# Optimization experiments

Measured on AMD Instinct MI355X. Metric: run time of the kernel, lower is better.

## Reference

```python
import jax, jax.numpy as jnp
import numpy as np

DIM = 256
NUM_HEADS = 4
HEAD_DIM = DIM // NUM_HEADS
SCALE = HEAD_DIM ** -0.5


def setup_inputs() -> dict:
    key = jax.random.key(0)
    ks = jax.random.split(key, 11)
    B, Nq, Nkv = 4, 2048, 2048
    inp = {
        "query_feat": jax.random.normal(ks[0], (B, Nq, DIM), dtype=jnp.float32),
        "key_value_feat": jax.random.normal(ks[1], (B, Nkv, DIM), dtype=jnp.float32),
        "reliability_kv": jax.random.uniform(ks[2], (B, Nkv), dtype=jnp.float32),
        "Wq": jax.random.normal(ks[3], (DIM, DIM), dtype=jnp.float32) * (DIM ** -0.5),
        "bq": jnp.zeros((DIM,), jnp.float32),
        "Wk": jax.random.normal(ks[4], (DIM, DIM), dtype=jnp.float32) * (DIM ** -0.5),
        "bk": jnp.zeros((DIM,), jnp.float32),
        "Wv": jax.random.normal(ks[5], (DIM, DIM), dtype=jnp.float32) * (DIM ** -0.5),
        "bv": jnp.zeros((DIM,), jnp.float32),
        "Wo": jax.random.normal(ks[6], (DIM, DIM), dtype=jnp.float32) * (DIM ** -0.5),
        "bo": jnp.zeros((DIM,), jnp.float32),
    }
    return inp


def _heads(x):
    B, N, C = x.shape
    return x.reshape(B, N, NUM_HEADS, HEAD_DIM).transpose(0, 2, 1, 3)  # [B,H,N,hd]


def reference(query_feat, key_value_feat, reliability_kv, Wq, bq, Wk, bk, Wv, bv, Wo, bo):
    B, Nq, _ = query_feat.shape
    q = _heads(query_feat @ Wq + bq)          # [B,H,Nq,hd]
    k = _heads(key_value_feat @ Wk + bk)      # [B,H,Nkv,hd]
    v = _heads(key_value_feat @ Wv + bv)
    # gate K/V by reliability (broadcast over heads and head_dim)
    rk = reliability_kv[:, None, :, None]     # [B,1,Nkv,1]
    k = k * rk
    v = v * rk
    attn = jnp.einsum("bhqd,bhkd->bhqk", q, k) * SCALE
    log_r = jnp.log(jnp.clip(reliability_kv, 1e-6))[:, None, None, :]  # [B,1,1,Nkv]
    attn = jax.nn.softmax(attn + log_r, axis=-1)  # [B,H,Nq,Nkv]
    out = jnp.einsum("bhqk,bhkd->bhqd", attn, v)
    out = out.transpose(0, 2, 1, 3).reshape(B, Nq, DIM)
    out = out @ Wo + bo
    attn_mean = attn.mean(axis=1)  # [B,Nq,Nkv]
    return out, attn_mean
```

## Files before the change

### kernel.cpp

```cpp
#include <hip/hip_runtime.h>


typedef __attribute__((ext_vector_type(8))) _Float16 half8;
typedef __attribute__((ext_vector_type(4))) float f32x4;

#define MFMAH(A, B, C) __builtin_amdgcn_mfma_f32_16x16x32_f16((A), (B), (C), 0, 0, 0)

__device__ __forceinline__ unsigned short f2h(float f) {
    union { _Float16 h; unsigned short u; } c; c.h = (_Float16)f; return c.u;
}
__device__ __forceinline__ float h2f(unsigned short u) {
    union { unsigned short u; _Float16 h; } c; c.u = u; return (float)c.h;
}
__device__ __forceinline__ half8 ldh8(const unsigned short* p) {
    return *reinterpret_cast<const half8*>(p);
}
__device__ __forceinline__ void gld16(const unsigned short* g, unsigned short* l) {
    __builtin_amdgcn_global_load_lds(
        (const __attribute__((address_space(1))) unsigned int*)g,
        (__attribute__((address_space(3))) unsigned int*)l, 16, 0, 0);
}

__global__ void wsplit_kernel(const float* __restrict__ Wq, const float* __restrict__ Wk,
                              const float* __restrict__ Wv, const float* __restrict__ Wo,
                              unsigned short* __restrict__ WT) {
    int e = blockIdx.x * 256 + threadIdx.x;
    int m = e >> 16;
    int idx = e & 65535;
    int k = idx >> 8, n = idx & 255;
    const float* W = (m == 0) ? Wq : (m == 1) ? Wk : (m == 2) ? Wv : Wo;
    WT[m * 65536 + n * 256 + k] = f2h(W[idx]);
}

#define STAGE_W(dst_, src_, kt_) do {                                               \
    _Pragma("unroll")                                                               \
    for (int j_ = 0; j_ < 4; ++j_) {                                                \
        int s_ = w * 4 + j_;                                                        \
        int rowl_ = 8 * s_ + (l >> 3);                                              \
        int so_ = rowl_ * 256 + (kt_) * 64 + (((l & 7) ^ (rowl_ & 7)) << 3);        \
        gld16(&(src_)[so_], &(dst_)[s_ * 512]);                                     \
    }                                                                               \
} while (0)

#define GEMM_TILE(buf_, kt_) do {                                                   \
    _Pragma("unroll")                                                               \
    for (int ksl_ = 0; ksl_ < 2; ++ksl_) {                                          \
        _Pragma("unroll")                                                           \
        for (int n_ = 0; n_ < 16; ++n_) {                                           \
            int r_ = n_ * 16 + l15;                                                 \
            int idx_ = r_ * 64 + ((((ksl_)*4 + lg) ^ (r_ & 7)) << 3);               \
            half8 b_ = ldh8(&(buf_)[idx_]);                                         \
            acc[n_] = MFMAH(ah[(kt_) * 2 + ksl_], b_, acc[n_]);                     \
        }                                                                           \
    }                                                                               \
} while (0)

__global__ __launch_bounds__(512, 1) void proj3_kernel(
    const float* __restrict__ query, const float* __restrict__ kv,
    const float* __restrict__ rel, const unsigned short* __restrict__ WT,
    const float* __restrict__ bq, const float* __restrict__ bk, const float* __restrict__ bv,
    unsigned short* __restrict__ Qh, unsigned short* __restrict__ Kh,
    unsigned short* __restrict__ Vtmp) {
    const int job = blockIdx.y;
    const float* X = (job == 0) ? query : kv;
    const unsigned short* wg = WT + job * 65536;
    const float* bias = (job == 0) ? bq : (job == 1) ? bk : bv;
    const float* rs = (job == 0) ? nullptr : rel;
    unsigned short* oh = (job == 0) ? Qh : (job == 1) ? Kh : Vtmp;

    __shared__ __align__(16) unsigned short wlds[2][256 * 64];

    const int w = threadIdx.x >> 6, l = threadIdx.x & 63;
    const int l15 = l & 15, lg = l >> 4;
    const int arow = blockIdx.x * 128 + w * 16 + l15;

    half8 ah[8];
#pragma unroll
    for (int ks = 0; ks < 8; ++ks) {
        const float* p = &X[arow * 256 + ks * 32 + lg * 8];
        float4 f0 = *reinterpret_cast<const float4*>(p);
        float4 f1 = *reinterpret_cast<const float4*>(p + 4);
        half8 t;
        t[0] = (_Float16)f0.x; t[1] = (_Float16)f0.y; t[2] = (_Float16)f0.z; t[3] = (_Float16)f0.w;
        t[4] = (_Float16)f1.x; t[5] = (_Float16)f1.y; t[6] = (_Float16)f1.z; t[7] = (_Float16)f1.w;
        ah[ks] = t;
    }
    f32x4 acc[16];
#pragma unroll
    for (int n = 0; n < 16; ++n) acc[n] = (f32x4){0.f, 0.f, 0.f, 0.f};

    STAGE_W(wlds[0], wg, 0);
    __syncthreads();
#pragma unroll
    for (int kt = 0; kt < 4; ++kt) {
        const int cur = kt & 1, nx = cur ^ 1;
        if (kt < 3) STAGE_W(wlds[nx], wg, kt + 1);
        GEMM_TILE(wlds[cur], kt);
        __syncthreads();
    }

    const int orow0 = blockIdx.x * 128 + w * 16 + lg * 4;
    float rsv[4];
#pragma unroll
    for (int r = 0; r < 4; ++r) rsv[r] = rs ? rs[orow0 + r] : 1.0f;
#pragma unroll
    for (int n = 0; n < 16; ++n) {
        const int col = n * 16 + l15;
        const float bn = bias[col];
#pragma unroll
        for (int r = 0; r < 4; ++r)
            oh[(orow0 + r) * 256 + col] = f2h((acc[n][r] + bn) * rsv[r]);
    }
}

__global__ void transpose_v_kernel(const unsigned short* __restrict__ Vtmp,
                                   unsigned short* __restrict__ Vt) {
    __shared__ unsigned short tile[32][36];
    const int b = blockIdx.z;
    const int k0 = blockIdx.x * 32, d0 = blockIdx.y * 32;
    const int t = threadIdx.x;
    {
        int kr = t >> 3, dc4 = (t & 7) * 4;
        ushort4 v = *reinterpret_cast<const ushort4*>(&Vtmp[(b * 2048 + k0 + kr) * 256 + d0 + dc4]);
        tile[kr][dc4 + 0] = v.x; tile[kr][dc4 + 1] = v.y;
        tile[kr][dc4 + 2] = v.z; tile[kr][dc4 + 3] = v.w;
    }
    __syncthreads();
    {
        int dr = t >> 3, kc4 = (t & 7) * 4;
        ushort4 o;
        o.x = tile[kc4 + 0][dr]; o.y = tile[kc4 + 1][dr];
        o.z = tile[kc4 + 2][dr]; o.w = tile[kc4 + 3][dr];
        *reinterpret_cast<ushort4*>(&Vt[(b * 256 + d0 + dr) * 2048 + k0 + kc4]) = o;
    }
}

__global__ __launch_bounds__(512, 1) void attn_pass1(
    const unsigned short* __restrict__ Qh, const unsigned short* __restrict__ Kh,
    const unsigned short* __restrict__ Vt, const float* __restrict__ rel,
    float* __restrict__ sinv_ws, unsigned short* __restrict__ AO) {
    const int bid = blockIdx.x;
    const int sw = (bid & 7) * 32 + (bid >> 3);
    const int b = sw >> 6;
    const int q0 = (sw & 63) * 32;
    const int tid = threadIdx.x;
    const int w = tid >> 6;
    const int h = w & 3, ks = w >> 2;
    const int l = tid & 63, l15 = l & 15, lg = l >> 4;
    const float C2 = 0.18033688011112042f;

    __shared__ __align__(16) unsigned short ldsK[8][2][2048];
    __shared__ __align__(16) unsigned short ldsV[8][2][2048];
    __shared__ __align__(16) unsigned short pbf[8][2][640];
    __shared__ __align__(16) unsigned short rel_h[2048];
    __shared__ float ssum_sh[2][4][2][16];

    {
        float4 v = reinterpret_cast<const float4*>(&rel[b * 2048])[tid];
        ushort4 o;
        o.x = f2h(fmaxf(v.x, 1e-6f)); o.y = f2h(fmaxf(v.y, 1e-6f));
        o.z = f2h(fmaxf(v.z, 1e-6f)); o.w = f2h(fmaxf(v.w, 1e-6f));
        *reinterpret_cast<ushort4*>(&rel_h[tid * 4]) = o;
    }

    half8 qf00, qf01, qf10, qf11;
    {
        const int o0 = (b * 2048 + q0 + l15) * 256 + h * 64 + lg * 8;
        const int o1 = (b * 2048 + q0 + 16 + l15) * 256 + h * 64 + lg * 8;
        qf00 = ldh8(&Qh[o0]); qf01 = ldh8(&Qh[o0 + 32]);
        qf10 = ldh8(&Qh[o1]); qf11 = ldh8(&Qh[o1 + 32]);
    }
    __syncthreads();

#define STAGE1(buf_, kt_) do {                                                      \
    _Pragma("unroll")                                                               \
    for (int j_ = 0; j_ < 4; ++j_) {                                                \
        int r_ = 8 * j_ + (l >> 3);                                                 \
        size_t sk_ = (size_t)(b * 2048 + (kt_) * 32 + r_) * 256 + h * 64 +          \
                     (((l & 7) ^ (l >> 3)) << 3);                                   \
        gld16(&Kh[sk_], &ldsK[w][buf_][j_ * 512]);                                  \
    }                                                                               \
    _Pragma("unroll")                                                               \
    for (int j_ = 0; j_ < 4; ++j_) {                                                \
        int d_ = 16 * j_ + (l >> 2);                                                \
        size_t sv_ = (size_t)(b * 256 + h * 64 + d_) * 2048 + (kt_) * 32 +          \
                     (((l & 3) ^ ((l >> 3) & 3)) << 3);                             \
        gld16(&Vt[sv_], &ldsV[w][buf_][j_ * 512]);                                  \
    }                                                                               \
} while (0)

    float ssum0 = 0.f, ssum1 = 0.f;
    f32x4 oacc0[4], oacc1[4];
#pragma unroll
    for (int dc = 0; dc < 4; ++dc) {
        oacc0[dc] = (f32x4){0.f, 0.f, 0.f, 0.f};
        oacc1[dc] = (f32x4){0.f, 0.f, 0.f, 0.f};
    }

    const int ktb = ks * 32;
    STAGE1(0, ktb);
    for (int i = 0; i < 32; ++i) {
        const int cur = i & 1, nx = cur ^ 1;
        if (i < 31) {
            STAGE1(nx, ktb + i + 1);
            asm volatile("s_waitcnt vmcnt(8)" ::: "memory");
        } else {
            asm volatile("s_waitcnt vmcnt(0)" ::: "memory");
        }
        __builtin_amdgcn_sched_barrier(0);
        const int kt = ktb + i;
#pragma unroll
        for (int kc = 0; kc < 2; ++kc) {
            const int r = kc * 16 + l15;
            const int rx = l15 & 7;
            half8 kf0 = ldh8(&ldsK[w][cur][r * 64 + ((lg ^ rx) << 3)]);
            half8 kf1 = ldh8(&ldsK[w][cur][r * 64 + (((4 + lg) ^ rx) << 3)]);
            f32x4 a0 = (f32x4){0.f, 0.f, 0.f, 0.f}, a1 = a0;
            a0 = MFMAH(kf0, qf00, a0); a0 = MFMAH(kf1, qf01, a0);
            a1 = MFMAH(kf0, qf10, a1); a1 = MFMAH(kf1, qf11, a1);
            float p00, p01, p02, p03, p10, p11, p12, p13;
            {
                const int kb0 = kt * 32 + kc * 16 + lg * 4;
                float rc0 = h2f(rel_h[kb0]),     rc1 = h2f(rel_h[kb0 + 1]);
                float rc2 = h2f(rel_h[kb0 + 2]), rc3 = h2f(rel_h[kb0 + 3]);
                p00 = exp2f(a0[0] * C2) * rc0; p01 = exp2f(a0[1] * C2) * rc1;
                p02 = exp2f(a0[2] * C2) * rc2; p03 = exp2f(a0[3] * C2) * rc3;
                p10 = exp2f(a1[0] * C2) * rc0; p11 = exp2f(a1[1] * C2) * rc1;
                p12 = exp2f(a1[2] * C2) * rc2; p13 = exp2f(a1[3] * C2) * rc3;
            }
            ssum0 += (p00 + p01) + (p02 + p03);
            ssum1 += (p10 + p11) + (p12 + p13);
            uint2 w0, w1;
            w0.x = (unsigned)f2h(p00) | ((unsigned)f2h(p01) << 16);
            w0.y = (unsigned)f2h(p02) | ((unsigned)f2h(p03) << 16);
            w1.x = (unsigned)f2h(p10) | ((unsigned)f2h(p11) << 16);
            w1.y = (unsigned)f2h(p12) | ((unsigned)f2h(p13) << 16);
            *reinterpret_cast<uint2*>(&pbf[w][0][l15 * 40 + kc * 16 + lg * 4]) = w0;
            *reinterpret_cast<uint2*>(&pbf[w][1][l15 * 40 + kc * 16 + lg * 4]) = w1;
        }
        {
            half8 pa0 = ldh8(&pbf[w][0][l15 * 40 + lg * 8]);
            half8 pa1 = ldh8(&pbf[w][1][l15 * 40 + lg * 8]);
#pragma unroll
            for (int dc = 0; dc < 4; ++dc) {
                const int d = dc * 16 + l15;
                half8 vf = ldh8(&ldsV[w][cur][d * 32 + ((lg ^ ((l15 >> 1) & 3)) << 3)]);
                oacc0[dc] = MFMAH(pa0, vf, oacc0[dc]);
                oacc1[dc] = MFMAH(pa1, vf, oacc1[dc]);
            }
        }
    }
#undef STAGE1

    {
        float v0 = ssum0, v1 = ssum1;
        v0 += __shfl_xor(v0, 16); v0 += __shfl_xor(v0, 32);
        v1 += __shfl_xor(v1, 16); v1 += __shfl_xor(v1, 32);
        if (lg == 0) {
            ssum_sh[ks][h][0][l15] = v0;
            ssum_sh[ks][h][1][l15] = v1;
        }
    }
    float* ob = (float*)&ldsV[4][0][0];
    if (ks == 1) {
        const int base = (h * 64 + l) * 32;
#pragma unroll
        for (int dc = 0; dc < 4; ++dc)
#pragma unroll
            for (int r4 = 0; r4 < 4; ++r4) {
                int i0 = dc * 4 + r4, i1 = 16 + dc * 4 + r4;
                ob[base + ((i0 + l) & 31)] = oacc0[dc][r4];
                ob[base + ((i1 + l) & 31)] = oacc1[dc][r4];
            }
    }
    __syncthreads();
    if (ks == 0) {
        const int base = (h * 64 + l) * 32;
        float siv0[4], siv1[4];
#pragma unroll
        for (int r4 = 0; r4 < 4; ++r4) {
            int q = lg * 4 + r4;
            siv0[r4] = 1.0f / (ssum_sh[0][h][0][q] + ssum_sh[1][h][0][q]);
            siv1[r4] = 1.0f / (ssum_sh[0][h][1][q] + ssum_sh[1][h][1][q]);
        }
#pragma unroll
        for (int dc = 0; dc < 4; ++dc)
#pragma unroll
            for (int r4 = 0; r4 < 4; ++r4) {
                int i0 = dc * 4 + r4, i1 = 16 + dc * 4 + r4;
                float t0 = (oacc0[dc][r4] + ob[base + ((i0 + l) & 31)]) * siv0[r4];
                float t1 = (oacc1[dc][r4] + ob[base + ((i1 + l) & 31)]) * siv1[r4];
                AO[(size_t)(b * 2048 + q0 + lg * 4 + r4) * 256 + h * 64 + dc * 16 + l15] = f2h(t0);
                AO[(size_t)(b * 2048 + q0 + 16 + lg * 4 + r4) * 256 + h * 64 + dc * 16 + l15] = f2h(t1);
            }
        if (l15 == 0) {
#pragma unroll
            for (int r4 = 0; r4 < 4; ++r4) {
                sinv_ws[(b * 4 + h) * 2048 + q0 + lg * 4 + r4] = siv0[r4];
                sinv_ws[(b * 4 + h) * 2048 + q0 + 16 + lg * 4 + r4] = siv1[r4];
            }
        }
    }
}

__global__ __launch_bounds__(256, 2) void attn_mean_kernel(
    const unsigned short* __restrict__ Qh, const unsigned short* __restrict__ Kh,
    const float* __restrict__ rel, const float* __restrict__ sinv_ws,
    float* __restrict__ attn_mean) {
    const int kslice = blockIdx.x >> 8;
    const int inner = blockIdx.x & 255;
    const int sw = (inner & 7) * 32 + (inner >> 3);
    const int b = sw >> 6;
    const int q0 = (sw & 63) * 32;
    const int tid = threadIdx.x;
    const int w = tid >> 6;
    const int h = w;
    const int l = tid & 63, l15 = l & 15, lg = l >> 4;
    const int kb = b * 2048;
    const float C2 = 0.18033688011112042f;

    __shared__ __align__(16) unsigned short ldsK[2][8192];
    __shared__ __align__(16) unsigned short pbf2[2][4][2][640];
    __shared__ __align__(16) unsigned short rel_h[2048];

#define STAGE_KM(dst_, kt_) do {                                                    \
    _Pragma("unroll")                                                               \
    for (int j_ = 0; j_ < 4; ++j_) {                                                \
        int s_ = w * 4 + j_;                                                        \
        int r_ = 2 * s_ + (l >> 5);                                                 \
        size_t so_ = (size_t)(kb + (kt_) * 32 + r_) * 256 +                         \
                     (((l & 31) ^ (r_ & 7)) << 3);                                  \
        gld16(&Kh[so_], &(dst_)[s_ * 512]);                                         \
    }                                                                               \
} while (0)

    {
        float4 v0 = reinterpret_cast<const float4*>(&rel[b * 2048])[tid * 2];
        float4 v1 = reinterpret_cast<const float4*>(&rel[b * 2048])[tid * 2 + 1];
        ushort4 o0, o1;
        o0.x = f2h(fmaxf(v0.x, 1e-6f)); o0.y = f2h(fmaxf(v0.y, 1e-6f));
        o0.z = f2h(fmaxf(v0.z, 1e-6f)); o0.w = f2h(fmaxf(v0.w, 1e-6f));
        o1.x = f2h(fmaxf(v1.x, 1e-6f)); o1.y = f2h(fmaxf(v1.y, 1e-6f));
        o1.z = f2h(fmaxf(v1.z, 1e-6f)); o1.w = f2h(fmaxf(v1.w, 1e-6f));
        *reinterpret_cast<ushort4*>(&rel_h[tid * 8]) = o0;
        *reinterpret_cast<ushort4*>(&rel_h[tid * 8 + 4]) = o1;
    }

    half8 qf00, qf01, qf10, qf11;
    {
        const int o0 = (b * 2048 + q0 + l15) * 256 + h * 64 + lg * 8;
        const int o1 = (b * 2048 + q0 + 16 + l15) * 256 + h * 64 + lg * 8;
        qf00 = ldh8(&Qh[o0]); qf01 = ldh8(&Qh[o0 + 32]);
        qf10 = ldh8(&Qh[o1]); qf11 = ldh8(&Qh[o1 + 32]);
    }
    const float si0 = sinv_ws[(b * 4 + h) * 2048 + q0 + l15];
    const float si1 = sinv_ws[(b * 4 + h) * 2048 + q0 + 16 + l15];

    const int kt0 = kslice * 16;
    STAGE_KM(ldsK[0], kt0);
    __syncthreads();
    for (int ki = 0; ki < 16; ++ki) {
        const int kt = kt0 + ki;
        const int cur = ki & 1, nx = cur ^ 1;
        if (ki < 15) STAGE_KM(ldsK[nx], kt + 1);
#pragma unroll
        for (int kc = 0; kc < 2; ++kc) {
            const int r = kc * 16 + l15;
            const int rx = r & 7;
            half8 kf0 = ldh8(&ldsK[cur][r * 256 + (((h * 8 + lg) ^ rx) << 3)]);
            half8 kf1 = ldh8(&ldsK[cur][r * 256 + (((h * 8 + 4 + lg) ^ rx) << 3)]);
            f32x4 a0 = (f32x4){0.f, 0.f, 0.f, 0.f}, a1 = a0;
            a0 = MFMAH(kf0, qf00, a0); a0 = MFMAH(kf1, qf01, a0);
            a1 = MFMAH(kf0, qf10, a1); a1 = MFMAH(kf1, qf11, a1);
            const int kb0 = kt * 32 + kc * 16 + lg * 4;
            float rc0 = h2f(rel_h[kb0]),     rc1 = h2f(rel_h[kb0 + 1]);
            float rc2 = h2f(rel_h[kb0 + 2]), rc3 = h2f(rel_h[kb0 + 3]);
            uint2 w0, w1;
            w0.x = (unsigned)f2h(exp2f(a0[0] * C2) * rc0 * si0) |
                   ((unsigned)f2h(exp2f(a0[1] * C2) * rc1 * si0) << 16);
            w0.y = (unsigned)f2h(exp2f(a0[2] * C2) * rc2 * si0) |
                   ((unsigned)f2h(exp2f(a0[3] * C2) * rc3 * si0) << 16);
            w1.x = (unsigned)f2h(exp2f(a1[0] * C2) * rc0 * si1) |
                   ((unsigned)f2h(exp2f(a1[1] * C2) * rc1 * si1) << 16);
            w1.y = (unsigned)f2h(exp2f(a1[2] * C2) * rc2 * si1) |
                   ((unsigned)f2h(exp2f(a1[3] * C2) * rc3 * si1) << 16);
            *reinterpret_cast<uint2*>(&pbf2[cur][h][0][l15 * 40 + kc * 16 + lg * 4]) = w0;
            *reinterpret_cast<uint2*>(&pbf2[cur][h][1][l15 * 40 + kc * 16 + lg * 4]) = w1;
        }
        __syncthreads();
        {
            const int qs_ = tid >> 7, row = (tid >> 3) & 15, kq = tid & 7;
            float m0 = 0.f, m1 = 0.f, m2 = 0.f, m3 = 0.f;
#pragma unroll
            for (int hh = 0; hh < 4; ++hh) {
                ushort4 u = *reinterpret_cast<const ushort4*>(&pbf2[cur][hh][qs_][row * 40 + kq * 4]);
                m0 += h2f(u.x); m1 += h2f(u.y); m2 += h2f(u.z); m3 += h2f(u.w);
            }
            float4 o = (float4){m0 * 0.25f, m1 * 0.25f, m2 * 0.25f, m3 * 0.25f};
            *reinterpret_cast<float4*>(
                &attn_mean[(size_t)(b * 2048 + q0 + qs_ * 16 + row) * 2048 + kt * 32 + kq * 4]) = o;
        }
    }
#undef STAGE_KM
}

__global__ __launch_bounds__(512, 1) void final_kernel(
    const unsigned short* __restrict__ AO, const unsigned short* __restrict__ WoT,
    const float* __restrict__ bo, float* __restrict__ out) {
    __shared__ __align__(16) unsigned short wlds[2][256 * 64];

    const int w = threadIdx.x >> 6, l = threadIdx.x & 63;
    const int l15 = l & 15, lg = l >> 4;
    const int arow = blockIdx.x * 128 + w * 16 + l15;

    half8 ah[8];
#pragma unroll
    for (int ks = 0; ks < 8; ++ks)
        ah[ks] = ldh8(&AO[arow * 256 + ks * 32 + lg * 8]);
    f32x4 acc[16];
#pragma unroll
    for (int n = 0; n < 16; ++n) acc[n] = (f32x4){0.f, 0.f, 0.f, 0.f};

    STAGE_W(wlds[0], WoT, 0);
    __syncthreads();
#pragma unroll
    for (int kt = 0; kt < 4; ++kt) {
        const int cur = kt & 1, nx = cur ^ 1;
        if (kt < 3) STAGE_W(wlds[nx], WoT, kt + 1);
        GEMM_TILE(wlds[cur], kt);
        __syncthreads();
    }

    const int orow0 = blockIdx.x * 128 + w * 16 + lg * 4;
#pragma unroll
    for (int n = 0; n < 16; ++n) {
        const int col = n * 16 + l15;
        const float bn = bo[col];
#pragma unroll
        for (int r = 0; r < 4; ++r)
            out[(orow0 + r) * 256 + col] = acc[n][r] + bn;
    }
}

extern "C" void kernel_launch(void* const* d_in, const int* in_sizes, int n_in,
                              void* d_out, int out_size, void* d_ws, size_t ws_size,
                              hipStream_t stream) {
    const float* query = (const float*)d_in[0];
    const float* kv    = (const float*)d_in[1];
    const float* rel   = (const float*)d_in[2];
    const float* Wq    = (const float*)d_in[3];
    const float* bq    = (const float*)d_in[4];
    const float* Wk    = (const float*)d_in[5];
    const float* bk    = (const float*)d_in[6];
    const float* Wv    = (const float*)d_in[7];
    const float* bv    = (const float*)d_in[8];
    const float* Wo    = (const float*)d_in[9];
    const float* bo    = (const float*)d_in[10];

    char* ws = (char*)d_ws;
    unsigned short* WT   = (unsigned short*)(ws + 0);
    unsigned short* Qh   = (unsigned short*)(ws + 524288);
    unsigned short* Kh   = (unsigned short*)(ws + 4718592);
    unsigned short* Vtmp = (unsigned short*)(ws + 8912896);
    unsigned short* Vt   = (unsigned short*)(ws + 13107200);
    unsigned short* AO   = (unsigned short*)(ws + 17301504);
    float*          sinv = (float*)(ws + 21495808);

    float* out = (float*)d_out;
    float* attn_mean = (float*)d_out + 2097152;

    wsplit_kernel<<<1024, 256, 0, stream>>>(Wq, Wk, Wv, Wo, WT);
    proj3_kernel<<<dim3(64, 3), 512, 0, stream>>>(query, kv, rel, WT,
                                                  bq, bk, bv, Qh, Kh, Vtmp);
    transpose_v_kernel<<<dim3(64, 8, 4), 256, 0, stream>>>(Vtmp, Vt);
    attn_pass1<<<256, 512, 0, stream>>>(Qh, Kh, Vt, rel, sinv, AO);
    attn_mean_kernel<<<1024, 256, 0, stream>>>(Qh, Kh, rel, sinv, attn_mean);
    final_kernel<<<64, 512, 0, stream>>>(AO, WT + 3 * 65536, bo, out);
}
```

Baseline: 129.3 us.

## Split attention KV range across blocks with combine kernel and restructure V layout

The attention pass now splits the KV range in two across blocks, doubling the grid to 512, writing fp32 partial outputs and row sums, and adds a combine kernel that reduces them into AO and the inverse sums. V is re-tiled into 16-key blocks so P can feed a 16x16x16 MFMA directly from registers, which removes the LDS round trip for P. Reliability is folded in as a precomputed log2 added inside exp2, with packed fp16 conversions. The attn_mean kernel is given finer k-slices and explicit waitcnt/barrier pipelining. The aim is more parallelism and less LDS traffic, at the cost of an extra kernel launch, the partial-output memory traffic, and reuse of the Vtmp buffer as scratch.

After: 123.1 us. -4.8%, faster.

```diff
diff --git a/kernel.cpp b/kernel.cpp
--- a/kernel.cpp
+++ b/kernel.cpp
@@ -2,9 +2,12 @@
 
 
 typedef __attribute__((ext_vector_type(8))) _Float16 half8;
+typedef __attribute__((ext_vector_type(4))) _Float16 half4;
+typedef __attribute__((ext_vector_type(2))) __fp16 fp16x2;
 typedef __attribute__((ext_vector_type(4))) float f32x4;
 
-#define MFMAH(A, B, C) __builtin_amdgcn_mfma_f32_16x16x32_f16((A), (B), (C), 0, 0, 0)
+#define MFMAH32(A, B, C) __builtin_amdgcn_mfma_f32_16x16x32_f16((A), (B), (C), 0, 0, 0)
+#define MFMAH16(A, B, C) __builtin_amdgcn_mfma_f32_16x16x16f16((A), (B), (C), 0, 0, 0)
 
 __device__ __forceinline__ unsigned short f2h(float f) {
     union { _Float16 h; unsigned short u; } c; c.h = (_Float16)f; return c.u;
@@ -14,6 +17,20 @@
 }
 __device__ __forceinline__ half8 ldh8(const unsigned short* p) {
     return *reinterpret_cast<const half8*>(p);
+}
+__device__ __forceinline__ half4 ldh4(const unsigned short* p) {
+    return *reinterpret_cast<const half4*>(p);
+}
+__device__ __forceinline__ half4 pk4(float a, float b, float c, float d) {
+    union { fp16x2 h2[2]; half4 h4; } u;
+    u.h2[0] = __builtin_amdgcn_cvt_pkrtz(a, b);
+    u.h2[1] = __builtin_amdgcn_cvt_pkrtz(c, d);
+    return u.h4;
+}
+__device__ __forceinline__ unsigned int pku(float a, float b) {
+    union { fp16x2 h2; unsigned int u; } c;
+    c.h2 = __builtin_amdgcn_cvt_pkrtz(a, b);
+    return c.u;
 }
 __device__ __forceinline__ void gld16(const unsigned short* g, unsigned short* l) {
     __builtin_amdgcn_global_load_lds(
@@ -50,7 +67,7 @@
             int r_ = n_ * 16 + l15;                                                 \
             int idx_ = r_ * 64 + ((((ksl_)*4 + lg) ^ (r_ & 7)) << 3);               \
             half8 b_ = ldh8(&(buf_)[idx_]);                                         \
-            acc[n_] = MFMAH(ah[(kt_) * 2 + ksl_], b_, acc[n_]);                     \
+            acc[n_] = MFMAH32(ah[(kt_) * 2 + ksl_], b_, acc[n_]);                   \
         }                                                                           \
     }                                                                               \
 } while (0)
@@ -115,192 +132,197 @@
 
 __global__ void transpose_v_kernel(const unsigned short* __restrict__ Vtmp,
                                    unsigned short* __restrict__ Vt) {
-    __shared__ unsigned short tile[32][36];
-    const int b = blockIdx.z;
-    const int k0 = blockIdx.x * 32, d0 = blockIdx.y * 32;
+    __shared__ unsigned short tile[16][264];
+    const int st = blockIdx.x, b = blockIdx.y;
     const int t = threadIdx.x;
+#pragma unroll
+    for (int it = 0; it < 4; ++it) {
+        int idx = it * 256 + t;
+        int kr = idx >> 6;
+        int d4 = (idx & 63) * 4;
+        ushort4 v = *reinterpret_cast<const ushort4*>(
+            &Vtmp[(size_t)(b * 2048 + st * 16 + kr) * 256 + d4]);
+        tile[kr][d4 + 0] = v.x; tile[kr][d4 + 1] = v.y;
+        tile[kr][d4 + 2] = v.z; tile[kr][d4 + 3] = v.w;
+    }
+    __syncthreads();
     {
-        int kr = t >> 3, dc4 = (t & 7) * 4;
-        ushort4 v = *reinterpret_cast<const ushort4*>(&Vtmp[(b * 2048 + k0 + kr) * 256 + d0 + dc4]);
-        tile[kr][dc4 + 0] = v.x; tile[kr][dc4 + 1] = v.y;
-        tile[kr][dc4 + 2] = v.z; tile[kr][dc4 + 3] = v.w;
-    }
-    __syncthreads();
-    {
-        int dr = t >> 3, kc4 = (t & 7) * 4;
-        ushort4 o;
-        o.x = tile[kc4 + 0][dr]; o.y = tile[kc4 + 1][dr];
-        o.z = tile[kc4 + 2][dr]; o.w = tile[kc4 + 3][dr];
-        *reinterpret_cast<ushort4*>(&Vt[(b * 256 + d0 + dr) * 2048 + k0 + kc4]) = o;
-    }
-}
-
-__global__ __launch_bounds__(512, 1) void attn_pass1(
+        const int d = t;
+        unsigned int u[8];
+#pragma unroll
+        for (int k2 = 0; k2 < 8; ++k2)
+            u[k2] = (unsigned int)tile[k2 * 2][d] | ((unsigned int)tile[k2 * 2 + 1][d] << 16);
+        uint4* dst = reinterpret_cast<uint4*>(&Vt[((size_t)(b * 128 + st) * 256 + d) * 16]);
+        dst[0] = (uint4){u[0], u[1], u[2], u[3]};
+        dst[1] = (uint4){u[4], u[5], u[6], u[7]};
+    }
+}
+
+__global__ __launch_bounds__(512, 4) void attn_pass1(
     const unsigned short* __restrict__ Qh, const unsigned short* __restrict__ Kh,
     const unsigned short* __restrict__ Vt, const float* __restrict__ rel,
-    float* __restrict__ sinv_ws, unsigned short* __restrict__ AO) {
+    float* __restrict__ po_a, float* __restrict__ po_b, float* __restrict__ ps) {
     const int bid = blockIdx.x;
-    const int sw = (bid & 7) * 32 + (bid >> 3);
-    const int b = sw >> 6;
-    const int q0 = (sw & 63) * 32;
+    const int sw = (bid & 7) * 64 + (bid >> 3);
+    const int b = sw >> 7;
+    const int rem = sw & 127;
+    const int kh = rem & 1;
+    const int q0 = (rem >> 1) * 32;
     const int tid = threadIdx.x;
-    const int w = tid >> 6;
-    const int h = w & 3, ks = w >> 2;
+    const int w = tid >> 6, h = w & 3, ks = w >> 2;
     const int l = tid & 63, l15 = l & 15, lg = l >> 4;
     const float C2 = 0.18033688011112042f;
 
-    __shared__ __align__(16) unsigned short ldsK[8][2][2048];
-    __shared__ __align__(16) unsigned short ldsV[8][2][2048];
-    __shared__ __align__(16) unsigned short pbf[8][2][640];
-    __shared__ __align__(16) unsigned short rel_h[2048];
+    __shared__ __align__(16) unsigned short ldsK[8][2][1024];
+    __shared__ __align__(16) unsigned short ldsV[8][2][1024];
+    __shared__ float rel_lr[2048];
     __shared__ float ssum_sh[2][4][2][16];
 
     {
         float4 v = reinterpret_cast<const float4*>(&rel[b * 2048])[tid];
-        ushort4 o;
-        o.x = f2h(fmaxf(v.x, 1e-6f)); o.y = f2h(fmaxf(v.y, 1e-6f));
-        o.z = f2h(fmaxf(v.z, 1e-6f)); o.w = f2h(fmaxf(v.w, 1e-6f));
-        *reinterpret_cast<ushort4*>(&rel_h[tid * 4]) = o;
+        float* d = &rel_lr[tid * 4];
+        d[0] = log2f(fmaxf(v.x, 1e-6f)); d[1] = log2f(fmaxf(v.y, 1e-6f));
+        d[2] = log2f(fmaxf(v.z, 1e-6f)); d[3] = log2f(fmaxf(v.w, 1e-6f));
     }
 
     half8 qf00, qf01, qf10, qf11;
     {
         const int o0 = (b * 2048 + q0 + l15) * 256 + h * 64 + lg * 8;
-        const int o1 = (b * 2048 + q0 + 16 + l15) * 256 + h * 64 + lg * 8;
+        const int o1 = o0 + 16 * 256;
         qf00 = ldh8(&Qh[o0]); qf01 = ldh8(&Qh[o0 + 32]);
         qf10 = ldh8(&Qh[o1]); qf11 = ldh8(&Qh[o1 + 32]);
     }
     __syncthreads();
 
-#define STAGE1(buf_, kt_) do {                                                      \
+    const int st0 = kh * 64 + ks * 32;
+
+#define STG(buf_, i_) do {                                                          \
+    const unsigned short* kbp_ = Kh + (size_t)(b * 2048 + (st0 + (i_)) * 16) * 256  \
+                                 + h * 64;                                          \
     _Pragma("unroll")                                                               \
-    for (int j_ = 0; j_ < 4; ++j_) {                                                \
-        int r_ = 8 * j_ + (l >> 3);                                                 \
-        size_t sk_ = (size_t)(b * 2048 + (kt_) * 32 + r_) * 256 + h * 64 +          \
-                     (((l & 7) ^ (l >> 3)) << 3);                                   \
-        gld16(&Kh[sk_], &ldsK[w][buf_][j_ * 512]);                                  \
+    for (int j_ = 0; j_ < 2; ++j_) {                                                \
+        int r_ = j_ * 8 + (l >> 3);                                                 \
+        gld16(kbp_ + r_ * 256 + (((l & 7) ^ ((l >> 3) & 7)) << 3),                  \
+              &ldsK[w][buf_][j_ * 512]);                                            \
     }                                                                               \
+    const unsigned short* vbp_ = Vt + (size_t)((b * 128 + st0 + (i_)) * 256         \
+                                 + h * 64) * 16;                                    \
     _Pragma("unroll")                                                               \
-    for (int j_ = 0; j_ < 4; ++j_) {                                                \
-        int d_ = 16 * j_ + (l >> 2);                                                \
-        size_t sv_ = (size_t)(b * 256 + h * 64 + d_) * 2048 + (kt_) * 32 +          \
-                     (((l & 3) ^ ((l >> 3) & 3)) << 3);                             \
-        gld16(&Vt[sv_], &ldsV[w][buf_][j_ * 512]);                                  \
+    for (int j_ = 0; j_ < 2; ++j_) {                                                \
+        int d_ = j_ * 32 + (l >> 1);                                                \
+        gld16(vbp_ + d_ * 16 + (((l & 1) ^ ((l >> 1) & 1)) << 3),                   \
+              &ldsV[w][buf_][j_ * 512]);                                            \
     }                                                                               \
 } while (0)
 
     float ssum0 = 0.f, ssum1 = 0.f;
-    f32x4 oacc0[4], oacc1[4];
+    f32x4 o0acc[4], o1acc[4];
 #pragma unroll
     for (int dc = 0; dc < 4; ++dc) {
-        oacc0[dc] = (f32x4){0.f, 0.f, 0.f, 0.f};
-        oacc1[dc] = (f32x4){0.f, 0.f, 0.f, 0.f};
-    }
-
-    const int ktb = ks * 32;
-    STAGE1(0, ktb);
+        o0acc[dc] = (f32x4){0.f, 0.f, 0.f, 0.f};
+        o1acc[dc] = (f32x4){0.f, 0.f, 0.f, 0.f};
+    }
+
+    STG(0, 0);
     for (int i = 0; i < 32; ++i) {
         const int cur = i & 1, nx = cur ^ 1;
         if (i < 31) {
-            STAGE1(nx, ktb + i + 1);
-            asm volatile("s_waitcnt vmcnt(8)" ::: "memory");
+            STG(nx, i + 1);
+            asm volatile("s_waitcnt vmcnt(4)" ::: "memory");
         } else {
             asm volatile("s_waitcnt vmcnt(0)" ::: "memory");
         }
         __builtin_amdgcn_sched_barrier(0);
-        const int kt = ktb + i;
-#pragma unroll
-        for (int kc = 0; kc < 2; ++kc) {
-            const int r = kc * 16 + l15;
-            const int rx = l15 & 7;
-            half8 kf0 = ldh8(&ldsK[w][cur][r * 64 + ((lg ^ rx) << 3)]);
-            half8 kf1 = ldh8(&ldsK[w][cur][r * 64 + (((4 + lg) ^ rx) << 3)]);
-            f32x4 a0 = (f32x4){0.f, 0.f, 0.f, 0.f}, a1 = a0;
-            a0 = MFMAH(kf0, qf00, a0); a0 = MFMAH(kf1, qf01, a0);
-            a1 = MFMAH(kf0, qf10, a1); a1 = MFMAH(kf1, qf11, a1);
-            float p00, p01, p02, p03, p10, p11, p12, p13;
-            {
-                const int kb0 = kt * 32 + kc * 16 + lg * 4;
-                float rc0 = h2f(rel_h[kb0]),     rc1 = h2f(rel_h[kb0 + 1]);
-                float rc2 = h2f(rel_h[kb0 + 2]), rc3 = h2f(rel_h[kb0 + 3]);
-                p00 = exp2f(a0[0] * C2) * rc0; p01 = exp2f(a0[1] * C2) * rc1;
-                p02 = exp2f(a0[2] * C2) * rc2; p03 = exp2f(a0[3] * C2) * rc3;
-                p10 = exp2f(a1[0] * C2) * rc0; p11 = exp2f(a1[1] * C2) * rc1;
-                p12 = exp2f(a1[2] * C2) * rc2; p13 = exp2f(a1[3] * C2) * rc3;
+        half8 kf0 = ldh8(&ldsK[w][cur][l15 * 64 + ((lg ^ (l15 & 7)) << 3)]);
+        half8 kf1 = ldh8(&ldsK[w][cur][l15 * 64 + (((4 + lg) ^ (l15 & 7)) << 3)]);
+        f32x4 a0 = (f32x4){0.f, 0.f, 0.f, 0.f}, a1 = a0;
+        a0 = MFMAH32(kf0, qf00, a0); a0 = MFMAH32(kf1, qf01, a0);
+        a1 = MFMAH32(kf0, qf10, a1); a1 = MFMAH32(kf1, qf11, a1);
+        float4 lr4 = *reinterpret_cast<const float4*>(&rel_lr[(st0 + i) * 16 + lg * 4]);
+        float p00 = exp2f(__builtin_fmaf(a0[0], C2, lr4.x));
+        float p01 = exp2f(__builtin_fmaf(a0[1], C2, lr4.y));
+        float p02 = exp2f(__builtin_fmaf(a0[2], C2, lr4.z));
+        float p03 = exp2f(__builtin_fmaf(a0[3], C2, lr4.w));
+        float p10 = exp2f(__builtin_fmaf(a1[0], C2, lr4.x));
+        float p11 = exp2f(__builtin_fmaf(a1[1], C2, lr4.y));
+        float p12 = exp2f(__builtin_fmaf(a1[2], C2, lr4.z));
+        float p13 = exp2f(__builtin_fmaf(a1[3], C2, lr4.w));
+        ssum0 += (p00 + p01) + (p02 + p03);
+        ssum1 += (p10 + p11) + (p12 + p13);
+        half4 pa0 = pk4(p00, p01, p02, p03);
+        half4 pa1 = pk4(p10, p11, p12, p13);
+#pragma unroll
+        for (int dc = 0; dc < 4; ++dc) {
+            const int d = dc * 16 + l15;
+            half4 vf = ldh4(&ldsV[w][cur][d * 16 + ((((lg >> 1) ^ (d & 1))) << 3) + (lg & 1) * 4]);
+            o0acc[dc] = MFMAH16(pa0, vf, o0acc[dc]);
+            o1acc[dc] = MFMAH16(pa1, vf, o1acc[dc]);
+        }
+    }
+#undef STG
+
+    float v0 = ssum0, v1 = ssum1;
+    v0 += __shfl_xor(v0, 16); v0 += __shfl_xor(v0, 32);
+    v1 += __shfl_xor(v1, 16); v1 += __shfl_xor(v1, 32);
+
+    __syncthreads();
+    if (l < 16) { ssum_sh[ks][h][0][l] = v0; ssum_sh[ks][h][1][l] = v1; }
+    float* obuf = (float*)&ldsK[0][0][0];
+    if (ks == 1) {
+#pragma unroll
+        for (int dc = 0; dc < 4; ++dc)
+#pragma unroll
+            for (int r = 0; r < 4; ++r) {
+                const int d = h * 64 + dc * 16 + l15;
+                obuf[(lg * 4 + r) * 256 + d] = o0acc[dc][r];
+                obuf[(16 + lg * 4 + r) * 256 + d] = o1acc[dc][r];
             }
-            ssum0 += (p00 + p01) + (p02 + p03);
-            ssum1 += (p10 + p11) + (p12 + p13);
-            uint2 w0, w1;
-            w0.x = (unsigned)f2h(p00) | ((unsigned)f2h(p01) << 16);
-            w0.y = (unsigned)f2h(p02) | ((unsigned)f2h(p03) << 16);
-            w1.x = (unsigned)f2h(p10) | ((unsigned)f2h(p11) << 16);
-            w1.y = (unsigned)f2h(p12) | ((unsigned)f2h(p13) << 16);
-            *reinterpret_cast<uint2*>(&pbf[w][0][l15 * 40 + kc * 16 + lg * 4]) = w0;
-            *reinterpret_cast<uint2*>(&pbf[w][1][l15 * 40 + kc * 16 + lg * 4]) = w1;
+    }
+    __syncthreads();
+    if (ks == 0) {
+        const int chunk = b * 2 + kh;
+        float* po = (chunk < 2) ? (po_a + (size_t)chunk * 524288)
+                                : (po_b + (size_t)(chunk - 2) * 524288);
+#pragma unroll
+        for (int dc = 0; dc < 4; ++dc)
+#pragma unroll
+            for (int r = 0; r < 4; ++r) {
+                const int d = h * 64 + dc * 16 + l15;
+                const int qa = lg * 4 + r, qb = 16 + lg * 4 + r;
+                po[(size_t)(q0 + qa) * 256 + d] = o0acc[dc][r] + obuf[qa * 256 + d];
+                po[(size_t)(q0 + qb) * 256 + d] = o1acc[dc][r] + obuf[qb * 256 + d];
+            }
+        if (l < 16) {
+            ps[(chunk * 4 + h) * 2048 + q0 + l] =
+                ssum_sh[0][h][0][l] + ssum_sh[1][h][0][l];
+            ps[(chunk * 4 + h) * 2048 + q0 + 16 + l] =
+                ssum_sh[0][h][1][l] + ssum_sh[1][h][1][l];
         }
-        {
-            half8 pa0 = ldh8(&pbf[w][0][l15 * 40 + lg * 8]);
-            half8 pa1 = ldh8(&pbf[w][1][l15 * 40 + lg * 8]);
-#pragma unroll
-            for (int dc = 0; dc < 4; ++dc) {
-                const int d = dc * 16 + l15;
-                half8 vf = ldh8(&ldsV[w][cur][d * 32 + ((lg ^ ((l15 >> 1) & 3)) << 3)]);
-                oacc0[dc] = MFMAH(pa0, vf, oacc0[dc]);
-                oacc1[dc] = MFMAH(pa1, vf, oacc1[dc]);
-            }
-        }
-    }
-#undef STAGE1
-
-    {
-        float v0 = ssum0, v1 = ssum1;
-        v0 += __shfl_xor(v0, 16); v0 += __shfl_xor(v0, 32);
-        v1 += __shfl_xor(v1, 16); v1 += __shfl_xor(v1, 32);
-        if (lg == 0) {
-            ssum_sh[ks][h][0][l15] = v0;
-            ssum_sh[ks][h][1][l15] = v1;
-        }
-    }
-    float* ob = (float*)&ldsV[4][0][0];
-    if (ks == 1) {
-        const int base = (h * 64 + l) * 32;
-#pragma unroll
-        for (int dc = 0; dc < 4; ++dc)
-#pragma unroll
-            for (int r4 = 0; r4 < 4; ++r4) {
-                int i0 = dc * 4 + r4, i1 = 16 + dc * 4 + r4;
-                ob[base + ((i0 + l) & 31)] = oacc0[dc][r4];
-                ob[base + ((i1 + l) & 31)] = oacc1[dc][r4];
-            }
-    }
-    __syncthreads();
-    if (ks == 0) {
-        const int base = (h * 64 + l) * 32;
-        float siv0[4], siv1[4];
-#pragma unroll
-        for (int r4 = 0; r4 < 4; ++r4) {
-            int q = lg * 4 + r4;
-            siv0[r4] = 1.0f / (ssum_sh[0][h][0][q] + ssum_sh[1][h][0][q]);
-            siv1[r4] = 1.0f / (ssum_sh[0][h][1][q] + ssum_sh[1][h][1][q]);
-        }
-#pragma unroll
-        for (int dc = 0; dc < 4; ++dc)
-#pragma unroll
-            for (int r4 = 0; r4 < 4; ++r4) {
-                int i0 = dc * 4 + r4, i1 = 16 + dc * 4 + r4;
-                float t0 = (oacc0[dc][r4] + ob[base + ((i0 + l) & 31)]) * siv0[r4];
-                float t1 = (oacc1[dc][r4] + ob[base + ((i1 + l) & 31)]) * siv1[r4];
-                AO[(size_t)(b * 2048 + q0 + lg * 4 + r4) * 256 + h * 64 + dc * 16 + l15] = f2h(t0);
-                AO[(size_t)(b * 2048 + q0 + 16 + lg * 4 + r4) * 256 + h * 64 + dc * 16 + l15] = f2h(t1);
-            }
-        if (l15 == 0) {
-#pragma unroll
-            for (int r4 = 0; r4 < 4; ++r4) {
-                sinv_ws[(b * 4 + h) * 2048 + q0 + lg * 4 + r4] = siv0[r4];
-                sinv_ws[(b * 4 + h) * 2048 + q0 + 16 + lg * 4 + r4] = siv1[r4];
-            }
-        }
-    }
+    }
+}
+
+__global__ __launch_bounds__(256) void combine_kernel(
+    const float* __restrict__ po_a, const float* __restrict__ po_b,
+    const float* __restrict__ ps, unsigned short* __restrict__ AO,
+    float* __restrict__ sinv_ws) {
+    const int t = blockIdx.x * 256 + threadIdx.x;
+    const int d4 = t & 63;
+    const int bq = t >> 6;
+    const int q = bq & 2047;
+    const int b = bq >> 11;
+    const int d0 = d4 * 4, h = d0 >> 6;
+    const int c0 = b * 2, c1 = b * 2 + 1;
+    const float* p0 = (c0 < 2) ? po_a + (size_t)c0 * 524288 : po_b + (size_t)(c0 - 2) * 524288;
+    const float* p1 = (c1 < 2) ? po_a + (size_t)c1 * 524288 : po_b + (size_t)(c1 - 2) * 524288;
+    float4 x = *reinterpret_cast<const float4*>(&p0[(size_t)q * 256 + d0]);
+    float4 y = *reinterpret_cast<const float4*>(&p1[(size_t)q * 256 + d0]);
+    float s = ps[(c0 * 4 + h) * 2048 + q] + ps[(c1 * 4 + h) * 2048 + q];
+    float si = 1.0f / s;
+    ushort4 o;
+    o.x = f2h((x.x + y.x) * si); o.y = f2h((x.y + y.y) * si);
+    o.z = f2h((x.z + y.z) * si); o.w = f2h((x.w + y.w) * si);
+    *reinterpret_cast<ushort4*>(&AO[((size_t)(b * 2048 + q)) * 256 + d0]) = o;
+    if (d4 == (h << 4)) sinv_ws[(b * 4 + h) * 2048 + q] = si;
 }
 
 __global__ __launch_bounds__(256, 2) void attn_mean_kernel(
@@ -321,7 +343,7 @@
 
     __shared__ __align__(16) unsigned short ldsK[2][8192];
     __shared__ __align__(16) unsigned short pbf2[2][4][2][640];
-    __shared__ __align__(16) unsigned short rel_h[2048];
+    __shared__ float rel_lr[2048];
 
 #define STAGE_KM(dst_, kt_) do {                                                    \
     _Pragma("unroll")                                                               \
@@ -337,32 +359,37 @@
     {
         float4 v0 = reinterpret_cast<const float4*>(&rel[b * 2048])[tid * 2];
         float4 v1 = reinterpret_cast<const float4*>(&rel[b * 2048])[tid * 2 + 1];
-        ushort4 o0, o1;
-        o0.x = f2h(fmaxf(v0.x, 1e-6f)); o0.y = f2h(fmaxf(v0.y, 1e-6f));
-        o0.z = f2h(fmaxf(v0.z, 1e-6f)); o0.w = f2h(fmaxf(v0.w, 1e-6f));
-        o1.x = f2h(fmaxf(v1.x, 1e-6f)); o1.y = f2h(fmaxf(v1.y, 1e-6f));
-        o1.z = f2h(fmaxf(v1.z, 1e-6f)); o1.w = f2h(fmaxf(v1.w, 1e-6f));
-        *reinterpret_cast<ushort4*>(&rel_h[tid * 8]) = o0;
-        *reinterpret_cast<ushort4*>(&rel_h[tid * 8 + 4]) = o1;
+        float* d = &rel_lr[tid * 8];
+        d[0] = log2f(fmaxf(v0.x, 1e-6f)); d[1] = log2f(fmaxf(v0.y, 1e-6f));
+        d[2] = log2f(fmaxf(v0.z, 1e-6f)); d[3] = log2f(fmaxf(v0.w, 1e-6f));
+        d[4] = log2f(fmaxf(v1.x, 1e-6f)); d[5] = log2f(fmaxf(v1.y, 1e-6f));
+        d[6] = log2f(fmaxf(v1.z, 1e-6f)); d[7] = log2f(fmaxf(v1.w, 1e-6f));
     }
 
     half8 qf00, qf01, qf10, qf11;
     {
         const int o0 = (b * 2048 + q0 + l15) * 256 + h * 64 + lg * 8;
-        const int o1 = (b * 2048 + q0 + 16 + l15) * 256 + h * 64 + lg * 8;
+        const int o1 = o0 + 16 * 256;
         qf00 = ldh8(&Qh[o0]); qf01 = ldh8(&Qh[o0 + 32]);
         qf10 = ldh8(&Qh[o1]); qf11 = ldh8(&Qh[o1 + 32]);
     }
-    const float si0 = sinv_ws[(b * 4 + h) * 2048 + q0 + l15];
-    const float si1 = sinv_ws[(b * 4 + h) * 2048 + q0 + 16 + l15];
-
-    const int kt0 = kslice * 16;
+    const float lsi0 = log2f(sinv_ws[(b * 4 + h) * 2048 + q0 + l15]) - 2.0f;
+    const float lsi1 = log2f(sinv_ws[(b * 4 + h) * 2048 + q0 + 16 + l15]) - 2.0f;
+    __syncthreads();
+
+    const int kt0 = kslice * 8;
     STAGE_KM(ldsK[0], kt0);
-    __syncthreads();
-    for (int ki = 0; ki < 16; ++ki) {
+    for (int ki = 0; ki < 8; ++ki) {
         const int kt = kt0 + ki;
         const int cur = ki & 1, nx = cur ^ 1;
-        if (ki < 15) STAGE_KM(ldsK[nx], kt + 1);
+        if (ki < 7) {
+            STAGE_KM(ldsK[nx], kt + 1);
+            asm volatile("s_waitcnt vmcnt(4)" ::: "memory");
+        } else {
+            asm volatile("s_waitcnt vmcnt(0)" ::: "memory");
+        }
+        asm volatile("s_barrier" ::: "memory");
+        __builtin_amdgcn_sched_barrier(0);
 #pragma unroll
         for (int kc = 0; kc < 2; ++kc) {
             const int r = kc * 16 + l15;
@@ -370,35 +397,37 @@
             half8 kf0 = ldh8(&ldsK[cur][r * 256 + (((h * 8 + lg) ^ rx) << 3)]);
             half8 kf1 = ldh8(&ldsK[cur][r * 256 + (((h * 8 + 4 + lg) ^ rx) << 3)]);
             f32x4 a0 = (f32x4){0.f, 0.f, 0.f, 0.f}, a1 = a0;
-            a0 = MFMAH(kf0, qf00, a0); a0 = MFMAH(kf1, qf01, a0);
-            a1 = MFMAH(kf0, qf10, a1); a1 = MFMAH(kf1, qf11, a1);
-            const int kb0 = kt * 32 + kc * 16 + lg * 4;
-            float rc0 = h2f(rel_h[kb0]),     rc1 = h2f(rel_h[kb0 + 1]);
-            float rc2 = h2f(rel_h[kb0 + 2]), rc3 = h2f(rel_h[kb0 + 3]);
+            a0 = MFMAH32(kf0, qf00, a0); a0 = MFMAH32(kf1, qf01, a0);
+            a1 = MFMAH32(kf0, qf10, a1); a1 = MFMAH32(kf1, qf11, a1);
+            float4 lr4 = *reinterpret_cast<const float4*>(
+                &rel_lr[kt * 32 + kc * 16 + lg * 4]);
+            float q00 = exp2f(__builtin_fmaf(a0[0], C2, lsi0) + lr4.x);
+            float q01 = exp2f(__builtin_fmaf(a0[1], C2, lsi0) + lr4.y);
+            float q02 = exp2f(__builtin_fmaf(a0[2], C2, lsi0) + lr4.z);
+            float q03 = exp2f(__builtin_fmaf(a0[3], C2, lsi0) + lr4.w);
+            float q10 = exp2f(__builtin_fmaf(a1[0], C2, lsi1) + lr4.x);
+            float q11 = exp2f(__builtin_fmaf(a1[1], C2, lsi1) + lr4.y);
+            float q12 = exp2f(__builtin_fmaf(a1[2], C2, lsi1) + lr4.z);
+            float q13 = exp2f(__builtin_fmaf(a1[3], C2, lsi1) + lr4.w);
             uint2 w0, w1;
-            w0.x = (unsigned)f2h(exp2f(a0[0] * C2) * rc0 * si0) |
-                   ((unsigned)f2h(exp2f(a0[1] * C2) * rc1 * si0) << 16);
-            w0.y = (unsigned)f2h(exp2f(a0[2] * C2) * rc2 * si0) |
-                   ((unsigned)f2h(exp2f(a0[3] * C2) * rc3 * si0) << 16);
-            w1.x = (unsigned)f2h(exp2f(a1[0] * C2) * rc0 * si1) |
-                   ((unsigned)f2h(exp2f(a1[1] * C2) * rc1 * si1) << 16);
-            w1.y = (unsigned)f2h(exp2f(a1[2] * C2) * rc2 * si1) |
-                   ((unsigned)f2h(exp2f(a1[3] * C2) * rc3 * si1) << 16);
+            w0.x = pku(q00, q01); w0.y = pku(q02, q03);
+            w1.x = pku(q10, q11); w1.y = pku(q12, q13);
             *reinterpret_cast<uint2*>(&pbf2[cur][h][0][l15 * 40 + kc * 16 + lg * 4]) = w0;
             *reinterpret_cast<uint2*>(&pbf2[cur][h][1][l15 * 40 + kc * 16 + lg * 4]) = w1;
         }
-        __syncthreads();
+        asm volatile("s_waitcnt lgkmcnt(0)\n\ts_barrier" ::: "memory");
         {
             const int qs_ = tid >> 7, row = (tid >> 3) & 15, kq = tid & 7;
             float m0 = 0.f, m1 = 0.f, m2 = 0.f, m3 = 0.f;
 #pragma unroll
             for (int hh = 0; hh < 4; ++hh) {
-                ushort4 u = *reinterpret_cast<const ushort4*>(&pbf2[cur][hh][qs_][row * 40 + kq * 4]);
+                ushort4 u = *reinterpret_cast<const ushort4*>(
+                    &pbf2[cur][hh][qs_][row * 40 + kq * 4]);
                 m0 += h2f(u.x); m1 += h2f(u.y); m2 += h2f(u.z); m3 += h2f(u.w);
             }
-            float4 o = (float4){m0 * 0.25f, m1 * 0.25f, m2 * 0.25f, m3 * 0.25f};
             *reinterpret_cast<float4*>(
-                &attn_mean[(size_t)(b * 2048 + q0 + qs_ * 16 + row) * 2048 + kt * 32 + kq * 4]) = o;
+                &attn_mean[(size_t)(b * 2048 + q0 + qs_ * 16 + row) * 2048 +
+                           kt * 32 + kq * 4]) = (float4){m0, m1, m2, m3};
         }
     }
 #undef STAGE_KM
@@ -465,6 +494,9 @@
     unsigned short* Vt   = (unsigned short*)(ws + 13107200);
     unsigned short* AO   = (unsigned short*)(ws + 17301504);
     float*          sinv = (float*)(ws + 21495808);
+    float*          ps   = (float*)(ws + 21626880);
+    float*          po_b = (float*)(ws + 21889024);
+    float*          po_a = (float*)Vtmp;
 
     float* out = (float*)d_out;
     float* attn_mean = (float*)d_out + 2097152;
@@ -472,8 +504,9 @@
     wsplit_kernel<<<1024, 256, 0, stream>>>(Wq, Wk, Wv, Wo, WT);
     proj3_kernel<<<dim3(64, 3), 512, 0, stream>>>(query, kv, rel, WT,
                                                   bq, bk, bv, Qh, Kh, Vtmp);
-    transpose_v_kernel<<<dim3(64, 8, 4), 256, 0, stream>>>(Vtmp, Vt);
-    attn_pass1<<<256, 512, 0, stream>>>(Qh, Kh, Vt, rel, sinv, AO);
-    attn_mean_kernel<<<1024, 256, 0, stream>>>(Qh, Kh, rel, sinv, attn_mean);
+    transpose_v_kernel<<<dim3(128, 4), 256, 0, stream>>>(Vtmp, Vt);
+    attn_pass1<<<512, 512, 0, stream>>>(Qh, Kh, Vt, rel, po_a, po_b, ps);
+    combine_kernel<<<2048, 256, 0, stream>>>(po_a, po_b, ps, AO, sinv);
+    attn_mean_kernel<<<2048, 256, 0, stream>>>(Qh, Kh, rel, sinv, attn_mean);
     final_kernel<<<64, 512, 0, stream>>>(AO, WT + 3 * 65536, bo, out);
 }
```
